# Kernel optimization log

Hardware: AMD Instinct MI355X
Metric: run time of the kernel (lower is better)

Reference implementation:

```python
import jax, jax.numpy as jnp
import numpy as np

B, S, D, H, DFF = 2, 2048, 1024, 16, 4096
DK = D // H
EPS = 1e-6


def setup_inputs() -> dict:
    key = jax.random.key(0)
    ks = jax.random.split(key, 12)
    p = lambda k, shp: (jax.random.normal(k, shp, dtype=jnp.float32) * 0.02)
    return {
        "x": jax.random.normal(ks[0], (B, S, D), dtype=jnp.float32),
        "src_mask": jax.random.randint(ks[1], (B, 1, 1, S), 0, 2, dtype=jnp.int32),
        "wq": p(ks[2], (D, D)), "bq": jnp.zeros((D,), jnp.float32),
        "wk": p(ks[3], (D, D)), "bk": jnp.zeros((D,), jnp.float32),
        "wv": p(ks[4], (D, D)), "bv": jnp.zeros((D,), jnp.float32),
        "wo": p(ks[5], (D, D)), "bo": jnp.zeros((D,), jnp.float32),
        "w1": p(ks[6], (D, DFF)), "b1": jnp.zeros((DFF,), jnp.float32),
        "w2": p(ks[7], (DFF, D)), "b2": jnp.zeros((D,), jnp.float32),
        "a1": jnp.ones((1,), jnp.float32), "g1": jnp.zeros((1,), jnp.float32),
        "a2": jnp.ones((1,), jnp.float32), "g2": jnp.zeros((1,), jnp.float32),
    }


def _layernorm(x, alpha, bias):
    # Faithful to source: scalar alpha/bias, std with Bessel correction, eps on std
    mean = jnp.mean(x, axis=-1, keepdims=True)
    std = jnp.std(x, axis=-1, keepdims=True, ddof=1)
    return alpha * (x - mean) / (std + EPS) + bias


def _encoder_block(x, src_mask, wq, bq, wk, bk, wv, bv, wo, bo,
                   w1, b1, w2, b2, a1, g1, a2, g2):
    # --- self-attention sublayer (pre-norm residual) ---
    n = _layernorm(x, a1, g1)
    q = (n @ wq + bq).reshape(B, S, H, DK)
    k = (n @ wk + bk).reshape(B, S, H, DK)
    v = (n @ wv + bv).reshape(B, S, H, DK)
    scores = jnp.einsum("bqhd,bkhd->bhqk", q, k) / jnp.sqrt(jnp.float32(DK))
    scores = jnp.where(src_mask == 0, jnp.float32(-1e9), scores)
    attn = jax.nn.softmax(scores, axis=-1)
    ctx = jnp.einsum("bhqk,bkhd->bqhd", attn, v).reshape(B, S, D)
    x = x + (ctx @ wo + bo)
    # --- feed-forward sublayer (pre-norm residual) ---
    n2 = _layernorm(x, a2, g2)
    ff = jax.nn.relu(n2 @ w1 + b1) @ w2 + b2
    return x + ff


def reference(x, src_mask, wq, bq, wk, bk, wv, bv, wo, bo,
              w1, b1, w2, b2, a1, g1, a2, g2):
    return _encoder_block(x, src_mask, wq, bq, wk, bk, wv, bv, wo, bo,
                          w1, b1, w2, b2, a1, g1, a2, g2)
```

## Files before the change

kernel.cpp:

```cpp
#include <hip/hip_runtime.h>
#include <hip/hip_bf16.h>
#include <cstdint>

constexpr int Bc  = 2;
constexpr int Sc  = 2048;
constexpr int Dc  = 1024;
constexpr int Hc  = 16;
constexpr int DKc = 64;
constexpr int DFFc= 4096;
constexpr int BSc = Bc * Sc;

typedef __attribute__((ext_vector_type(8))) short bf16x8;
typedef __attribute__((ext_vector_type(4))) float f32x4;

__device__ __forceinline__ unsigned short f2bf(float x){
  union { float f; uint32_t u; } v; v.f = x;
  uint32_t r = v.u + 0x7fffu + ((v.u >> 16) & 1u);
  return (unsigned short)(r >> 16);
}

__device__ __forceinline__ void gload16(const void* g, void* l){
  __builtin_amdgcn_global_load_lds((const __attribute__((address_space(1))) void*)g,
                                   (__attribute__((address_space(3))) void*)l, 16, 0, 0);
}

__device__ __forceinline__ f32x4 mfma16(bf16x8 a, bf16x8 b, f32x4 c){
  return __builtin_amdgcn_mfma_f32_16x16x32_bf16(a, b, c, 0, 0, 0);
}

__device__ __forceinline__ uint32_t pk2bf(float lo, float hi){
  __hip_bfloat162 h = __float22bfloat162_rn(make_float2(lo, hi));
  return *reinterpret_cast<uint32_t*>(&h);
}

__device__ __forceinline__ float fexp2(float x){
  float r; asm("v_exp_f32 %0, %1" : "=v"(r) : "v"(x)); return r;
}

__device__ __forceinline__ int xcd_swz(int bid, int nwg){
  const int q = nwg >> 3, r = nwg & 7;
  const int xcd = bid & 7, idx = bid >> 3;
  return ((xcd < r) ? (xcd * (q + 1)) : (r * (q + 1) + (xcd - r) * q)) + idx;
}

__global__ __launch_bounds__(256)
void transpose_w(const float* __restrict__ in, unsigned short* __restrict__ out,
                 int K, int N){
  __shared__ float t[32][33];
  const int tx = threadIdx.x, ty = threadIdx.y;
  const int x0 = blockIdx.x * 32, y0 = blockIdx.y * 32;
#pragma unroll
  for (int j = ty; j < 32; j += 8) t[j][tx] = in[(long)(y0 + j) * N + x0 + tx];
  __syncthreads();
#pragma unroll
  for (int j = ty; j < 32; j += 8)
    out[(long)(x0 + j) * K + y0 + tx] = f2bf(t[tx][j]);
}

__global__ __launch_bounds__(256)
void concat_bias(const float* __restrict__ bq, const float* __restrict__ bk,
                 const float* __restrict__ bv, float* __restrict__ bqkv){
  int i = blockIdx.x * 256 + threadIdx.x;
  float v = (i < 1024) ? bq[i] : (i < 2048 ? bk[i - 1024] : bv[i - 2048]);
  bqkv[i] = v;
}

__global__ __launch_bounds__(256)
void mask_addend(const int* __restrict__ mask, float* __restrict__ madd){
  int i = blockIdx.x * 256 + threadIdx.x;
  madd[i] = (mask[i] != 0) ? 0.f : -1.442695e9f;
}

__global__ __launch_bounds__(256)
void layernorm_k(const float* __restrict__ x, const float* __restrict__ al,
                 const float* __restrict__ be, unsigned short* __restrict__ out){
  const int row = blockIdx.x, tid = threadIdx.x;
  const float4 v = ((const float4*)(x + (long)row * Dc))[tid];
  float s  = v.x + v.y + v.z + v.w;
  float ss = v.x*v.x + v.y*v.y + v.z*v.z + v.w*v.w;
#pragma unroll
  for (int d = 1; d < 64; d <<= 1){ s += __shfl_xor(s, d, 64); ss += __shfl_xor(ss, d, 64); }
  __shared__ float red[8];
  const int wid = tid >> 6, lane = tid & 63;
  if (lane == 0){ red[wid*2] = s; red[wid*2+1] = ss; }
  __syncthreads();
  s  = red[0] + red[2] + red[4] + red[6];
  ss = red[1] + red[3] + red[5] + red[7];
  const float mean = s * (1.f / 1024.f);
  float var = (ss - s * mean) * (1.f / 1023.f);
  var = fmaxf(var, 0.f);
  const float k = al[0] / (sqrtf(var) + 1e-6f);
  const float g = be[0];
  ushort4 o;
  o.x = f2bf((v.x - mean) * k + g);
  o.y = f2bf((v.y - mean) * k + g);
  o.z = f2bf((v.z - mean) * k + g);
  o.w = f2bf((v.w - mean) * k + g);
  ((ushort4*)(out + (long)row * Dc))[tid] = o;
}

template<int RELU, int OUTBF16, int RES>
__global__ __launch_bounds__(512, 2)
void gemm256(const unsigned short* __restrict__ A, const unsigned short* __restrict__ BT,
             const float* __restrict__ bias, const float* __restrict__ resid,
             void* __restrict__ Cout, int M, int N, int K){
  __shared__ unsigned short As[2][256 * 64];
  __shared__ unsigned short Bs[2][256 * 64];
  const int tid = threadIdx.x, wid = tid >> 6, lane = tid & 63;
  const int lg = lane >> 4, lr = lane & 15;
  const int wm = wid >> 2, wn = wid & 3;
  const int nwg = gridDim.x * gridDim.y;
  const int wg  = xcd_swz(blockIdx.y * gridDim.x + blockIdx.x, nwg);
  const int bx = wg % gridDim.x, by = wg / gridDim.x;
  const int m0 = by * 256, n0 = bx * 256;
  const long ldA = (long)K * 2;
  const f32x4 zero4 = {0.f, 0.f, 0.f, 0.f};
  f32x4 acc[8][4];
#pragma unroll
  for (int i = 0; i < 8; i++)
#pragma unroll
    for (int j = 0; j < 4; j++) acc[i][j] = zero4;

  auto stage_half = [&](int b, int kt, int h){
    const unsigned short* src = (h < 2) ? A : BT;
    const int rowg = ((h < 2) ? m0 : n0) + (h & 1) * 128;
    char* dst = ((h < 2) ? (char*)As[b] : (char*)Bs[b]) + (h & 1) * 16384;
#pragma unroll
    for (int l = 0; l < 2; ++l){
      const int ob = (wid*2 + l) * 1024;
      const int o  = ob + lane * 16;
      const int rr = o >> 7, c = (o >> 4) & 7;
      const long co = (long)kt * 128 + ((c ^ (rr & 7)) << 4);
      gload16((const char*)src + (long)(rowg + rr) * ldA + co, dst + ob);
    }
  };

  const int nt = K >> 6;
#pragma unroll
  for (int h = 0; h < 4; ++h) stage_half(0, 0, h);
  __syncthreads();

  int cur = 0;
  for (int t = 0; t < nt; ++t){
    const char* as = (const char*)As[cur];
    const char* bs = (const char*)Bs[cur];
    bf16x8 bfr[4][2];
#pragma unroll
    for (int p = 0; p < 4; ++p){
      if (p == 0){
#pragma unroll
        for (int ni = 0; ni < 4; ++ni){
          const int row = wn*64 + ni*16 + lr;
#pragma unroll
          for (int ks = 0; ks < 2; ++ks)
            bfr[ni][ks] = *reinterpret_cast<const bf16x8*>(bs + row*128 + (((ks*4 + lg) ^ (row & 7)) << 4));
        }
      }
      bf16x8 af[2][2];
#pragma unroll
      for (int i = 0; i < 2; ++i){
        const int arow = wm*128 + (2*p + i)*16 + lr;
        af[i][0] = *reinterpret_cast<const bf16x8*>(as + arow*128 + (((0*4 + lg) ^ (arow & 7)) << 4));
        af[i][1] = *reinterpret_cast<const bf16x8*>(as + arow*128 + (((1*4 + lg) ^ (arow & 7)) << 4));
      }
      if (t + 1 < nt) stage_half(cur ^ 1, t + 1, p);
      __builtin_amdgcn_sched_barrier(0);
      __builtin_amdgcn_s_barrier();
      asm volatile("s_waitcnt lgkmcnt(0)" ::: "memory");
      __builtin_amdgcn_sched_barrier(0);
      __builtin_amdgcn_s_setprio(1);
#pragma unroll
      for (int i = 0; i < 2; ++i){
        const int mi = 2*p + i;
#pragma unroll
        for (int ni = 0; ni < 4; ++ni){
          acc[mi][ni] = mfma16(af[i][0], bfr[ni][0], acc[mi][ni]);
          acc[mi][ni] = mfma16(af[i][1], bfr[ni][1], acc[mi][ni]);
        }
      }
      __builtin_amdgcn_s_setprio(0);
      __builtin_amdgcn_sched_barrier(0);
      __builtin_amdgcn_s_barrier();
    }
    if (t + 1 < nt){
      asm volatile("s_waitcnt vmcnt(0)" ::: "memory");
      __builtin_amdgcn_s_barrier();
      __builtin_amdgcn_sched_barrier(0);
    }
    cur ^= 1;
  }

#pragma unroll
  for (int mi = 0; mi < 8; ++mi)
#pragma unroll
    for (int ni = 0; ni < 4; ++ni){
      const int col = n0 + wn*64 + ni*16 + lr;
      const float bc = bias[col];
#pragma unroll
      for (int r = 0; r < 4; ++r){
        const int row = m0 + wm*128 + mi*16 + lg*4 + r;
        float v = acc[mi][ni][r] + bc;
        if (RES)  v += resid[(long)row * N + col];
        if (RELU) v = fmaxf(v, 0.f);
        if (OUTBF16) ((unsigned short*)Cout)[(long)row * N + col] = f2bf(v);
        else         ((float*)Cout)[(long)row * N + col] = v;
      }
    }
}

template<int RELU, int OUTBF16, int RES, int PARTIAL>
__global__ __launch_bounds__(512, 2)
void gemm128(const unsigned short* __restrict__ A, const unsigned short* __restrict__ BT,
             const float* __restrict__ bias, const float* __restrict__ resid,
             void* __restrict__ Cout, float* __restrict__ p0,
             float* __restrict__ p1a, float* __restrict__ p1b,
             int M, int N, int K, int ldK){
  __shared__ unsigned short As[2][128 * 64];
  __shared__ unsigned short Bs[2][128 * 64];
  const int tid = threadIdx.x, wid = tid >> 6, lane = tid & 63;
  const int lg = lane >> 4, lr = lane & 15;
  const int wm = wid >> 2, wn = wid & 3;
  const int nwg = gridDim.x * gridDim.y;
  const int wg  = xcd_swz(blockIdx.y * gridDim.x + blockIdx.x, nwg);
  const int bx = wg % gridDim.x, by = wg / gridDim.x;
  const int m0 = by * 128, n0 = bx * 128;
  const int kc = PARTIAL ? blockIdx.z : 0;
  const unsigned short* Ab = A  + (long)kc * K;
  const unsigned short* Bb = BT + (long)kc * K;
  const long ldA = (long)ldK * 2;
  const f32x4 zero4 = {0.f, 0.f, 0.f, 0.f};
  f32x4 acc[4][2];
#pragma unroll
  for (int i = 0; i < 4; i++)
#pragma unroll
    for (int j = 0; j < 2; j++) acc[i][j] = zero4;

  auto stage = [&](int b, int kt){
#pragma unroll
    for (int l = 0; l < 2; ++l){
      const int ob = (wid*2 + l) * 1024;
      const int o  = ob + lane * 16;
      const int rr = o >> 7, c = (o >> 4) & 7;
      const long co = (long)kt * 128 + ((c ^ (rr & 7)) << 4);
      gload16((const char*)Ab + (long)(m0 + rr) * ldA + co, (char*)As[b] + ob);
      gload16((const char*)Bb + (long)(n0 + rr) * ldA + co, (char*)Bs[b] + ob);
    }
  };

  const int nt = K >> 6;
  stage(0, 0);
  stage(1, 1);

  int cur = 0;
  for (int t = 0; t < nt; ++t){
    if (t + 1 < nt) asm volatile("s_waitcnt vmcnt(4)" ::: "memory");
    else            asm volatile("s_waitcnt vmcnt(0)" ::: "memory");
    __builtin_amdgcn_s_barrier();
    __builtin_amdgcn_sched_barrier(0);
    const char* as = (const char*)As[cur];
    const char* bs = (const char*)Bs[cur];
    bf16x8 bfr[2][2];
#pragma unroll
    for (int ni = 0; ni < 2; ++ni){
      const int row = wn*32 + ni*16 + lr;
#pragma unroll
      for (int ks = 0; ks < 2; ++ks)
        bfr[ni][ks] = *reinterpret_cast<const bf16x8*>(bs + row*128 + (((ks*4 + lg) ^ (row & 7)) << 4));
    }
    __builtin_amdgcn_s_setprio(1);
#pragma unroll
    for (int mi = 0; mi < 4; ++mi){
      const int arow = wm*64 + mi*16 + lr;
      bf16x8 a0 = *reinterpret_cast<const bf16x8*>(as + arow*128 + (((0*4 + lg) ^ (arow & 7)) << 4));
      bf16x8 a1 = *reinterpret_cast<const bf16x8*>(as + arow*128 + (((1*4 + lg) ^ (arow & 7)) << 4));
#pragma unroll
      for (int ni = 0; ni < 2; ++ni){
        acc[mi][ni] = mfma16(a0, bfr[ni][0], acc[mi][ni]);
        acc[mi][ni] = mfma16(a1, bfr[ni][1], acc[mi][ni]);
      }
    }
    __builtin_amdgcn_s_setprio(0);
    __builtin_amdgcn_s_barrier();
    __builtin_amdgcn_sched_barrier(0);
    if (t + 2 < nt) stage(cur, t + 2);
    cur ^= 1;
  }

#pragma unroll
  for (int mi = 0; mi < 4; ++mi)
#pragma unroll
    for (int ni = 0; ni < 2; ++ni){
      const int col = n0 + wn*32 + ni*16 + lr;
      float bc = 0.f;
      if (!PARTIAL) bc = bias[col];
#pragma unroll
      for (int r = 0; r < 4; ++r){
        const int row = m0 + wm*64 + mi*16 + lg*4 + r;
        float v = acc[mi][ni][r] + bc;
        if (PARTIAL){
          float* pb = (kc == 0) ? p0 : ((row < 2048) ? p1a : (p1b - 2097152));
          pb[(long)row * N + col] = v;
        } else {
          if (RES)  v += resid[(long)row * N + col];
          if (RELU) v = fmaxf(v, 0.f);
          if (OUTBF16) ((unsigned short*)Cout)[(long)row * N + col] = f2bf(v);
          else         ((float*)Cout)[(long)row * N + col] = v;
        }
      }
    }
}

__global__ __launch_bounds__(256)
void reduce_ff2(const float* __restrict__ p0, const float* __restrict__ p1a,
                const float* __restrict__ p1b, const float* __restrict__ b2,
                float* __restrict__ out){
  const long n4 = (long)BSc * Dc / 4;
  for (long i = (long)blockIdx.x * 256 + threadIdx.x; i < n4; i += (long)gridDim.x * 256){
    const long flat = i * 4;
    const float4 a = ((const float4*)p0)[i];
    const float4 b = (flat < 2097152L) ? ((const float4*)p1a)[i]
                                       : ((const float4*)p1b)[i - 524288L];
    const float4 x = ((const float4*)out)[i];
    const float4 bb = ((const float4*)b2)[(flat & 1023) >> 2];
    float4 r;
    r.x = a.x + b.x + x.x + bb.x;
    r.y = a.y + b.y + x.y + bb.y;
    r.z = a.z + b.z + x.z + bb.z;
    r.w = a.w + b.w + x.w + bb.w;
    ((float4*)out)[i] = r;
  }
}

__global__ __launch_bounds__(256)
void transpose_v(const unsigned short* __restrict__ qkv, unsigned short* __restrict__ vt){
  __shared__ unsigned short tile[64][72];
  const int st = blockIdx.x * 64, bh = blockIdx.y;
  const int b = bh >> 4, h = bh & 15;
  const int tid = threadIdx.x;
  const int r = tid >> 2, c0 = (tid & 3) * 16;
  const unsigned short* src = qkv + ((long)(b*Sc + st + r) * 3072 + 2048 + h*64 + c0);
  *(uint4*)&tile[r][c0]     = *(const uint4*)src;
  *(uint4*)&tile[r][c0 + 8] = *(const uint4*)(src + 8);
  __syncthreads();
  union { unsigned short u[8]; uint4 v; } w0, w1;
#pragma unroll
  for (int j = 0; j < 8; j++){ w0.u[j] = tile[c0 + j][r]; w1.u[j] = tile[c0 + 8 + j][r]; }
  unsigned short* dst = vt + ((long)(bh*64 + r) * Sc + st + c0);
  *(uint4*)dst       = w0.v;
  *(uint4*)(dst + 8) = w1.v;
}

__global__ __launch_bounds__(512)
void attn_k(const unsigned short* __restrict__ qkv, const unsigned short* __restrict__ vt,
            const float* __restrict__ madd, unsigned short* __restrict__ ctx){
  __shared__ unsigned short Qs[128*64], Ks[2][64*64], Vs[2][64*64], Ps[8*16*64];
  const int tid = threadIdx.x, wid = tid >> 6, lane = tid & 63;
  const int lg = lane >> 4, lr = lane & 15;
  const int f   = blockIdx.y * gridDim.x + blockIdx.x;
  const int xcd = f & 7, j = f >> 3;
  const int bh  = (xcd << 2) | (j & 3);
  const int qt  = j >> 2;
  const int b = bh >> 4, h = bh & 15;
  const int s0 = qt * 128;
  const f32x4 zero4 = {0.f, 0.f, 0.f, 0.f};
  const short onebf = (short)0x3F80;
  const bf16x8 ones = {onebf, onebf, onebf, onebf, onebf, onebf, onebf, onebf};
  const float c1 = 0.18033688f;

  const char* kbase = (const char*)qkv + (long)(b*Sc) * 6144 + 2048 + h * 128;
  const char* vbase = (const char*)vt + (long)bh * 64 * 4096;
  const float* mrow = madd + b * Sc;
  unsigned short* pb = Ps + wid * 1024;

  auto stageKV = [&](int t, int bsel){
    const int o = wid * 1024;
    const int ol = o + lane * 16;
    const int r = ol >> 7, c = (ol >> 4) & 7;
    const int sw = ((c ^ (r & 7)) << 4);
    gload16(kbase + (long)(t*64 + r) * 6144 + sw, (char*)Ks[bsel] + o);
    gload16(vbase + (long)r * 4096 + t*128 + sw, (char*)Vs[bsel] + o);
  };

  const char* qbase = (const char*)qkv + ((long)(b*Sc + s0)) * 6144 + h * 128;
#pragma unroll
  for (int ld = 0; ld < 2; ++ld){
    const int o = (wid*2 + ld) * 1024;
    const int ol = o + lane * 16;
    const int r = ol >> 7, c = (ol >> 4) & 7;
    gload16(qbase + (long)r * 6144 + ((c ^ (r & 7)) << 4), (char*)Qs + o);
  }
  stageKV(0, 0);
  float4 ma[4];
#pragma unroll
  for (int ni = 0; ni < 4; ++ni) ma[ni] = *(const float4*)(mrow + ni*16 + lg*4);
  __syncthreads();
  bf16x8 qb[2];
#pragma unroll
  for (int ks = 0; ks < 2; ++ks){
    const int row = wid*16 + lr;
    qb[ks] = *reinterpret_cast<const bf16x8*>((const char*)Qs + row*128 + (((ks*4 + lg) ^ (row & 7)) << 4));
  }

  f32x4 acc[4] = {zero4, zero4, zero4, zero4};
  f32x4 accS = zero4;
  constexpr int NT = Sc / 64;

  for (int t = 0; t < NT; ++t){
    if (t){
      asm volatile("s_waitcnt vmcnt(0)" ::: "memory");
      __builtin_amdgcn_s_barrier();
      __builtin_amdgcn_sched_barrier(0);
    }
    if (t + 1 < NT) stageKV(t + 1, (t + 1) & 1);
    float4 man[4];
    if (t + 1 < NT){
#pragma unroll
      for (int ni = 0; ni < 4; ++ni) man[ni] = *(const float4*)(mrow + (t+1)*64 + ni*16 + lg*4);
    }

    const int cur = t & 1;
    const char* ksb = (const char*)Ks[cur];
    const char* vsb = (const char*)Vs[cur];

    f32x4 s4[4];
    __builtin_amdgcn_s_setprio(1);
#pragma unroll
    for (int ni = 0; ni < 4; ++ni){
      s4[ni] = zero4;
      const int row = ni*16 + lr;
#pragma unroll
      for (int ks = 0; ks < 2; ++ks){
        bf16x8 ak = *reinterpret_cast<const bf16x8*>(ksb + row*128 + (((ks*4 + lg) ^ (lr & 7)) << 4));
        s4[ni] = mfma16(ak, qb[ks], s4[ni]);
      }
    }
    __builtin_amdgcn_s_setprio(0);

    float p[4][4];
#pragma unroll
    for (int ni = 0; ni < 4; ++ni){
      p[ni][0] = fexp2(fmaf(s4[ni][0], c1, ma[ni].x));
      p[ni][1] = fexp2(fmaf(s4[ni][1], c1, ma[ni].y));
      p[ni][2] = fexp2(fmaf(s4[ni][2], c1, ma[ni].z));
      p[ni][3] = fexp2(fmaf(s4[ni][3], c1, ma[ni].w));
    }

#pragma unroll
    for (int ni = 0; ni < 4; ++ni){
      uint2 w;
      w.x = pk2bf(p[ni][0], p[ni][1]);
      w.y = pk2bf(p[ni][2], p[ni][3]);
      const int c = ni*2 + (lg >> 1);
      char* dst = (char*)pb + lr*128 + ((c ^ (lr & 7)) << 4) + (lg & 1) * 8;
      *(uint2*)dst = w;
    }
    bf16x8 pa[2];
#pragma unroll
    for (int ks = 0; ks < 2; ++ks){
      pa[ks] = *reinterpret_cast<const bf16x8*>((const char*)pb + lr*128 + (((ks*4 + lg) ^ (lr & 7)) << 4));
    }
    __builtin_amdgcn_s_setprio(1);
#pragma unroll
    for (int ks = 0; ks < 2; ++ks) accS = mfma16(pa[ks], ones, accS);
#pragma unroll
    for (int ni = 0; ni < 4; ++ni){
      const int row = ni*16 + lr;
#pragma unroll
      for (int ks = 0; ks < 2; ++ks){
        bf16x8 bv8 = *reinterpret_cast<const bf16x8*>(vsb + row*128 + (((ks*4 + lg) ^ (lr & 7)) << 4));
        acc[ni] = mfma16(pa[ks], bv8, acc[ni]);
      }
    }
    __builtin_amdgcn_s_setprio(0);
    if (t + 1 < NT){
#pragma unroll
      for (int ni = 0; ni < 4; ++ni) ma[ni] = man[ni];
    }
  }
#pragma unroll
  for (int ni = 0; ni < 4; ++ni){
    const int col = h*64 + ni*16 + lr;
#pragma unroll
    for (int r = 0; r < 4; ++r){
      const int row = s0 + wid*16 + lg*4 + r;
      ctx[(long)(b*Sc + row) * Dc + col] = f2bf(acc[ni][r] / accS[r]);
    }
  }
}

extern "C" void kernel_launch(void* const* d_in, const int* in_sizes, int n_in,
                              void* d_out, int out_size, void* d_ws, size_t ws_size,
                              hipStream_t stream){
  const float* x  = (const float*)d_in[0];
  const int* mask = (const int*)d_in[1];
  const float* wq = (const float*)d_in[2];
  const float* bq = (const float*)d_in[3];
  const float* wk = (const float*)d_in[4];
  const float* bk = (const float*)d_in[5];
  const float* wv = (const float*)d_in[6];
  const float* bv = (const float*)d_in[7];
  const float* wo = (const float*)d_in[8];
  const float* bo = (const float*)d_in[9];
  const float* w1 = (const float*)d_in[10];
  const float* b1 = (const float*)d_in[11];
  const float* w2 = (const float*)d_in[12];
  const float* b2 = (const float*)d_in[13];
  const float* a1 = (const float*)d_in[14];
  const float* g1 = (const float*)d_in[15];
  const float* a2 = (const float*)d_in[16];
  const float* g2 = (const float*)d_in[17];

  if (ws_size < 75509760u) return;

  char* ws = (char*)d_ws;
  unsigned short* wqkv_t = (unsigned short*)(ws + 0);
  unsigned short* wo_t   = (unsigned short*)(ws + 6291456);
  unsigned short* w1_t   = (unsigned short*)(ws + 8388608);
  unsigned short* w2_t   = (unsigned short*)(ws + 16777216);
  float*          bqkv   = (float*)(ws + 25165824);
  unsigned short* nbuf   = (unsigned short*)(ws + 25178112);
  float*          maddf  = (float*)(ws + 25178112);
  unsigned short* qkv    = (unsigned short*)(ws + 33566720);
  unsigned short* ff1    = (unsigned short*)(ws + 33566720);
  unsigned short* vt     = (unsigned short*)(ws + 58732544);
  unsigned short* ctx    = (unsigned short*)(ws + 67121152);
  float* p0  = (float*)(ws + 0);
  float* p1a = (float*)(ws + 25178112);
  float* p1b = (float*)(ws + 67121152);
  float* x2 = (float*)d_out;

  const dim3 tb(32, 8);
  transpose_w<<<dim3(32, 32),  tb, 0, stream>>>(wq, wqkv_t,            1024, 1024);
  transpose_w<<<dim3(32, 32),  tb, 0, stream>>>(wk, wqkv_t + 1048576,  1024, 1024);
  transpose_w<<<dim3(32, 32),  tb, 0, stream>>>(wv, wqkv_t + 2097152,  1024, 1024);
  transpose_w<<<dim3(32, 32),  tb, 0, stream>>>(wo, wo_t,              1024, 1024);
  transpose_w<<<dim3(128, 32), tb, 0, stream>>>(w1, w1_t,              1024, 4096);
  transpose_w<<<dim3(32, 128), tb, 0, stream>>>(w2, w2_t,              4096, 1024);
  concat_bias<<<12, 256, 0, stream>>>(bq, bk, bv, bqkv);

  layernorm_k<<<BSc, 256, 0, stream>>>(x, a1, g1, nbuf);
  gemm256<0,1,0><<<dim3(12, 16), 512, 0, stream>>>(nbuf, wqkv_t, bqkv, nullptr, qkv, BSc, 3072, 1024);
  mask_addend<<<16, 256, 0, stream>>>(mask, maddf);
  transpose_v<<<dim3(32, 32), 256, 0, stream>>>(qkv, vt);
  attn_k<<<dim3(16, 32), 512, 0, stream>>>(qkv, vt, maddf, ctx);
  gemm128<0,0,1,0><<<dim3(8, 32), 512, 0, stream>>>(ctx, wo_t, bo, x, x2,
                                                    nullptr, nullptr, nullptr, BSc, 1024, 1024, 1024);
  layernorm_k<<<BSc, 256, 0, stream>>>(x2, a2, g2, nbuf);
  gemm256<1,1,0><<<dim3(16, 16), 512, 0, stream>>>(nbuf, w1_t, b1, nullptr, ff1, BSc, 4096, 1024);
  gemm128<0,0,0,1><<<dim3(8, 32, 2), 512, 0, stream>>>(ff1, w2_t, nullptr, nullptr, nullptr,
                                                       p0, p1a, p1b, BSc, 1024, 2048, 4096);
  reduce_ff2<<<2048, 256, 0, stream>>>(p0, p1a, p1b, b2, (float*)d_out);
}
```

Measured before the change: 237.2 us.

## Fuse weight prep into one kernel and write transposed V from QKV GEMM

Six weight-transpose launches and the bias concat are merged into a single prep_all kernel that dispatches on block index, cutting launch overhead. The QKV GEMM epilogue now writes the V columns straight into the transposed vt layout, so the separate transpose_v kernel and its extra read and write of V are removed. The V epilogue stores 4 consecutive sequence positions per lane as ushort4, a strided write pattern that may coalesce less well than the old tiled transpose.

```diff
diff --git a/kernel.cpp b/kernel.cpp
--- a/kernel.cpp
+++ b/kernel.cpp
@@ -44,25 +44,42 @@
 }
 
 __global__ __launch_bounds__(256)
-void transpose_w(const float* __restrict__ in, unsigned short* __restrict__ out,
-                 int K, int N){
+void prep_all(const float* __restrict__ wq, const float* __restrict__ wk,
+              const float* __restrict__ wv, const float* __restrict__ wo,
+              const float* __restrict__ w1, const float* __restrict__ w2,
+              const float* __restrict__ bq, const float* __restrict__ bk,
+              const float* __restrict__ bv,
+              unsigned short* __restrict__ wqkv_t, unsigned short* __restrict__ wo_t,
+              unsigned short* __restrict__ w1_t, unsigned short* __restrict__ w2_t,
+              float* __restrict__ bqkv){
+  const int id = blockIdx.x, tid = threadIdx.x;
+  if (id >= 12288){
+    const int i = (id - 12288) * 256 + tid;
+    bqkv[i] = (i < 1024) ? bq[i] : (i < 2048 ? bk[i - 1024] : bv[i - 2048]);
+    return;
+  }
+  const float* in; unsigned short* out; int K, N, bx, by;
+  if (id < 4096){
+    const int w = id >> 10, local = id & 1023;
+    in  = (w == 0) ? wq : (w == 1) ? wk : (w == 2) ? wv : wo;
+    out = (w == 0) ? wqkv_t : (w == 1) ? (wqkv_t + 1048576) : (w == 2) ? (wqkv_t + 2097152) : wo_t;
+    K = 1024; N = 1024; bx = local & 31; by = local >> 5;
+  } else if (id < 8192){
+    const int local = id - 4096;
+    in = w1; out = w1_t; K = 1024; N = 4096; bx = local & 127; by = local >> 7;
+  } else {
+    const int local = id - 8192;
+    in = w2; out = w2_t; K = 4096; N = 1024; bx = local & 31; by = local >> 5;
+  }
   __shared__ float t[32][33];
-  const int tx = threadIdx.x, ty = threadIdx.y;
-  const int x0 = blockIdx.x * 32, y0 = blockIdx.y * 32;
+  const int tx = tid & 31, ty = tid >> 5;
+  const int x0 = bx * 32, y0 = by * 32;
 #pragma unroll
   for (int j = ty; j < 32; j += 8) t[j][tx] = in[(long)(y0 + j) * N + x0 + tx];
   __syncthreads();
 #pragma unroll
   for (int j = ty; j < 32; j += 8)
     out[(long)(x0 + j) * K + y0 + tx] = f2bf(t[tx][j]);
-}
-
-__global__ __launch_bounds__(256)
-void concat_bias(const float* __restrict__ bq, const float* __restrict__ bk,
-                 const float* __restrict__ bv, float* __restrict__ bqkv){
-  int i = blockIdx.x * 256 + threadIdx.x;
-  float v = (i < 1024) ? bq[i] : (i < 2048 ? bk[i - 1024] : bv[i - 2048]);
-  bqkv[i] = v;
 }
 
 __global__ __launch_bounds__(256)
@@ -99,11 +116,12 @@
   ((ushort4*)(out + (long)row * Dc))[tid] = o;
 }
 
-template<int RELU, int OUTBF16, int RES>
+template<int RELU, int OUTBF16, int RES, int VOUT>
 __global__ __launch_bounds__(512, 2)
 void gemm256(const unsigned short* __restrict__ A, const unsigned short* __restrict__ BT,
              const float* __restrict__ bias, const float* __restrict__ resid,
-             void* __restrict__ Cout, int M, int N, int K){
+             void* __restrict__ Cout, unsigned short* __restrict__ vtw,
+             int M, int N, int K){
   __shared__ unsigned short As[2][256 * 64];
   __shared__ unsigned short Bs[2][256 * 64];
   const int tid = threadIdx.x, wid = tid >> 6, lane = tid & 63;
@@ -188,6 +206,26 @@
       __builtin_amdgcn_sched_barrier(0);
     }
     cur ^= 1;
+  }
+
+  if (VOUT && n0 >= 2048){
+#pragma unroll
+    for (int mi = 0; mi < 8; ++mi){
+      const int row = m0 + wm*128 + mi*16 + lg*4;
+      const int b = row >> 11, s = row & 2047;
+#pragma unroll
+      for (int ni = 0; ni < 4; ++ni){
+        const int col = n0 + wn*64 + ni*16 + lr;
+        const float bc = bias[col];
+        ushort4 o;
+        o.x = f2bf(acc[mi][ni][0] + bc);
+        o.y = f2bf(acc[mi][ni][1] + bc);
+        o.z = f2bf(acc[mi][ni][2] + bc);
+        o.w = f2bf(acc[mi][ni][3] + bc);
+        *(ushort4*)(vtw + ((long)(b * 1024 + (col - 2048)) << 11) + s) = o;
+      }
+    }
+    return;
   }
 
 #pragma unroll
@@ -331,25 +369,6 @@
   }
 }
 
-__global__ __launch_bounds__(256)
-void transpose_v(const unsigned short* __restrict__ qkv, unsigned short* __restrict__ vt){
-  __shared__ unsigned short tile[64][72];
-  const int st = blockIdx.x * 64, bh = blockIdx.y;
-  const int b = bh >> 4, h = bh & 15;
-  const int tid = threadIdx.x;
-  const int r = tid >> 2, c0 = (tid & 3) * 16;
-  const unsigned short* src = qkv + ((long)(b*Sc + st + r) * 3072 + 2048 + h*64 + c0);
-  *(uint4*)&tile[r][c0]     = *(const uint4*)src;
-  *(uint4*)&tile[r][c0 + 8] = *(const uint4*)(src + 8);
-  __syncthreads();
-  union { unsigned short u[8]; uint4 v; } w0, w1;
-#pragma unroll
-  for (int j = 0; j < 8; j++){ w0.u[j] = tile[c0 + j][r]; w1.u[j] = tile[c0 + 8 + j][r]; }
-  unsigned short* dst = vt + ((long)(bh*64 + r) * Sc + st + c0);
-  *(uint4*)dst       = w0.v;
-  *(uint4*)(dst + 8) = w1.v;
-}
-
 __global__ __launch_bounds__(512)
 void attn_k(const unsigned short* __restrict__ qkv, const unsigned short* __restrict__ vt,
             const float* __restrict__ madd, unsigned short* __restrict__ ctx){
@@ -529,24 +548,17 @@
   float* p1b = (float*)(ws + 67121152);
   float* x2 = (float*)d_out;
 
-  const dim3 tb(32, 8);
-  transpose_w<<<dim3(32, 32),  tb, 0, stream>>>(wq, wqkv_t,            1024, 1024);
-  transpose_w<<<dim3(32, 32),  tb, 0, stream>>>(wk, wqkv_t + 1048576,  1024, 1024);
-  transpose_w<<<dim3(32, 32),  tb, 0, stream>>>(wv, wqkv_t + 2097152,  1024, 1024);
-  transpose_w<<<dim3(32, 32),  tb, 0, stream>>>(wo, wo_t,              1024, 1024);
-  transpose_w<<<dim3(128, 32), tb, 0, stream>>>(w1, w1_t,              1024, 4096);
-  transpose_w<<<dim3(32, 128), tb, 0, stream>>>(w2, w2_t,              4096, 1024);
-  concat_bias<<<12, 256, 0, stream>>>(bq, bk, bv, bqkv);
+  prep_all<<<12300, 256, 0, stream>>>(wq, wk, wv, wo, w1, w2, bq, bk, bv,
+                                      wqkv_t, wo_t, w1_t, w2_t, bqkv);
 
   layernorm_k<<<BSc, 256, 0, stream>>>(x, a1, g1, nbuf);
-  gemm256<0,1,0><<<dim3(12, 16), 512, 0, stream>>>(nbuf, wqkv_t, bqkv, nullptr, qkv, BSc, 3072, 1024);
+  gemm256<0,1,0,1><<<dim3(12, 16), 512, 0, stream>>>(nbuf, wqkv_t, bqkv, nullptr, qkv, vt, BSc, 3072, 1024);
   mask_addend<<<16, 256, 0, stream>>>(mask, maddf);
-  transpose_v<<<dim3(32, 32), 256, 0, stream>>>(qkv, vt);
   attn_k<<<dim3(16, 32), 512, 0, stream>>>(qkv, vt, maddf, ctx);
   gemm128<0,0,1,0><<<dim3(8, 32), 512, 0, stream>>>(ctx, wo_t, bo, x, x2,
                                                     nullptr, nullptr, nullptr, BSc, 1024, 1024, 1024);
   layernorm_k<<<BSc, 256, 0, stream>>>(x2, a2, g2, nbuf);
-  gemm256<1,1,0><<<dim3(16, 16), 512, 0, stream>>>(nbuf, w1_t, b1, nullptr, ff1, BSc, 4096, 1024);
+  gemm256<1,1,0,0><<<dim3(16, 16), 512, 0, stream>>>(nbuf, w1_t, b1, nullptr, ff1, nullptr, BSc, 4096, 1024);
   gemm128<0,0,0,1><<<dim3(8, 32, 2), 512, 0, stream>>>(ff1, w2_t, nullptr, nullptr, nullptr,
                                                        p0, p1a, p1b, BSc, 1024, 2048, 4096);
   reduce_ff2<<<2048, 256, 0, stream>>>(p0, p1a, p1b, b2, (float*)d_out);
```

Measured after the change: 222.4 us. 1.07x faster.
